# Performance work log

Hardware: AMD Instinct MI355X
Metric: run time of the kernel (lower is better)

The kernel has to match this reference:

```python
import jax, jax.numpy as jnp
import numpy as np
from functools import partial

D_MODEL, D_STATE, D_CONV, EXPAND = 1024, 16, 4, 2
D_INNER = D_MODEL * EXPAND
B_SZ, L = 4, 2048


def setup_inputs() -> dict:
    key = jax.random.key(0)
    ks = jax.random.split(key, 8)
    s = 0.02
    A_init = jnp.log(jnp.arange(1, D_STATE + 1, dtype=jnp.float32))
    return {
        "x": jax.random.normal(ks[0], (B_SZ, L, D_MODEL), jnp.float32),
        "norm_w": jnp.ones((D_MODEL,), jnp.float32),
        "norm_b": jnp.zeros((D_MODEL,), jnp.float32),
        "W_in": jax.random.normal(ks[1], (D_MODEL, 2 * D_INNER), jnp.float32) * s,
        "conv_w": jax.random.normal(ks[2], (D_INNER, 1, D_CONV), jnp.float32) * 0.3,
        "conv_b": jnp.zeros((D_INNER,), jnp.float32),
        "A_log": jnp.broadcast_to(A_init, (D_INNER, D_STATE)).copy(),
        "W_b": jax.random.normal(ks[3], (D_INNER, D_STATE), jnp.float32) * s,
        "W_c": jax.random.normal(ks[4], (D_INNER, D_STATE), jnp.float32) * s,
        "W_delta": jax.random.normal(ks[5], (D_INNER, D_INNER), jnp.float32) * s,
        "b_delta": jnp.zeros((D_INNER,), jnp.float32),
        "D_param": jnp.ones((D_INNER,), jnp.float32),
        "W_out": jax.random.normal(ks[6], (D_INNER, D_MODEL), jnp.float32) * s,
    }


def _layernorm(x, w, b, eps=1e-5):
    mu = jnp.mean(x, axis=-1, keepdims=True)
    var = jnp.mean(jnp.square(x - mu), axis=-1, keepdims=True)
    return (x - mu) * jax.lax.rsqrt(var + eps) * w + b


def reference(x, norm_w, norm_b, W_in, conv_w, conv_b, A_log, W_b, W_c,
              W_delta, b_delta, D_param, W_out):
    residual = x
    xn = _layernorm(x, norm_w, norm_b)
    xz = jnp.einsum('bld,de->ble', xn, W_in)  # [B, L, 2*D_inner]
    x_path, z = jnp.split(xz, 2, axis=-1)

    # depthwise causal conv1d (torch pads both sides K-1 then slices [:L] == left-pad K-1)
    xc = jnp.moveaxis(x_path, 1, 2)  # [B, D_inner, L]
    xc = jax.lax.conv_general_dilated(
        xc, conv_w, window_strides=(1,), padding=[(D_CONV - 1, 0)],
        dimension_numbers=('NCH', 'OIH', 'NCH'), feature_group_count=D_INNER)
    xc = xc + conv_b[None, :, None]
    x_path = jax.nn.silu(jnp.moveaxis(xc, 2, 1))  # [B, L, D_inner]

    Bm = jnp.einsum('bld,dn->bln', x_path, W_b)   # [B, L, N]
    Cm = jnp.einsum('bld,dn->bln', x_path, W_c)   # [B, L, N]
    delta = jax.nn.softplus(jnp.einsum('bld,de->ble', x_path, W_delta) + b_delta)
    A = -jnp.exp(A_log)  # [D_inner, N]

    def step(h, inp):
        xt, dt, Bt, Ct = inp  # xt,dt: [B,D]; Bt,Ct: [B,N]
        A_bar = jnp.exp(dt[..., None] * A)              # [B, D, N]
        h = A_bar * h + (dt * xt)[..., None] * Bt[:, None, :]
        y = jnp.einsum('bdn,bn->bd', h, Ct) + D_param * xt
        return h, y

    h0 = jnp.zeros((x.shape[0], D_INNER, D_STATE), x_path.dtype)
    xs = (jnp.moveaxis(x_path, 1, 0), jnp.moveaxis(delta, 1, 0),
          jnp.moveaxis(Bm, 1, 0), jnp.moveaxis(Cm, 1, 0))
    _, ys = jax.lax.scan(step, h0, xs)           # ys: [L, B, D_inner]
    y = jnp.moveaxis(ys, 0, 1)                   # [B, L, D_inner]

    return jnp.einsum('bld,de->ble', y * jax.nn.silu(z), W_out) + residual
```

## Files before the change

### kernel.cpp

```cpp
#include <hip/hip_runtime.h>
#include <hip/hip_bf16.h>

#define D_MODEL 1024
#define D_STATE 16
#define D_INNER 2048
#define BSZ     4
#define SEQ     2048
#define NTOK    (BSZ*SEQ)
#define NCH     16
#define TC      128

typedef __attribute__((ext_vector_type(8))) short short8;
typedef __attribute__((ext_vector_type(4))) float floatx4;

__device__ __forceinline__ ushort bf2us(float f)
{
    union { __hip_bfloat16 h; ushort u; } c;
    c.h = __float2bfloat16(f);
    return c.u;
}
__device__ __forceinline__ float us2f(ushort u)
{
    union { uint u; float f; } c;
    c.u = ((uint)u) << 16;
    return c.f;
}
__device__ __forceinline__ uint pk2(float a, float b)
{
    return (uint)bf2us(a) | ((uint)bf2us(b) << 16);
}
__device__ __forceinline__ float blo(uint u) { return __uint_as_float(u << 16); }
__device__ __forceinline__ float bhi(uint u) { return __uint_as_float(u & 0xffff0000u); }
__device__ __forceinline__ float softplus_f(float v)
{
    return (v > 20.f) ? v : __logf(1.f + __expf(v));
}

__device__ __forceinline__ void load_lds16(const __hip_bfloat16* g, __hip_bfloat16* l)
{
    __builtin_amdgcn_global_load_lds(
        (const __attribute__((address_space(1))) char*)g,
        (__attribute__((address_space(3))) char*)l, 16, 0, 0);
}

__global__ __launch_bounds__(256) void ln_kernel(
    const float* __restrict__ x, const float* __restrict__ w,
    const float* __restrict__ bvec, __hip_bfloat16* __restrict__ out)
{
    int token = blockIdx.x;
    int tid = threadIdx.x;
    const float4 v = ((const float4*)(x + (size_t)token * D_MODEL))[tid];
    float s  = v.x + v.y + v.z + v.w;
    float sq = v.x*v.x + v.y*v.y + v.z*v.z + v.w*v.w;
#pragma unroll
    for (int o = 32; o; o >>= 1) { s += __shfl_down(s, o, 64); sq += __shfl_down(sq, o, 64); }
    __shared__ float red[8];
    int wid = tid >> 6;
    if ((tid & 63) == 0) { red[wid] = s; red[wid + 4] = sq; }
    __syncthreads();
    s  = red[0] + red[1] + red[2] + red[3];
    sq = red[4] + red[5] + red[6] + red[7];
    float mu  = s * (1.f / D_MODEL);
    float var = sq * (1.f / D_MODEL) - mu * mu;
    float rs  = rsqrtf(var + 1e-5f);
    float4 wv = ((const float4*)w)[tid];
    float4 bv = ((const float4*)bvec)[tid];
    union { ushort4 u; __hip_bfloat16 h[4]; } p;
    p.h[0] = __float2bfloat16((v.x - mu) * rs * wv.x + bv.x);
    p.h[1] = __float2bfloat16((v.y - mu) * rs * wv.y + bv.y);
    p.h[2] = __float2bfloat16((v.z - mu) * rs * wv.z + bv.z);
    p.h[3] = __float2bfloat16((v.w - mu) * rs * wv.w + bv.w);
    ((ushort4*)(out + (size_t)token * D_MODEL))[tid] = p.u;
}

__device__ __forceinline__ void tr_body(
    const float* __restrict__ src, __hip_bfloat16* __restrict__ dst,
    int R, int C, int dstStride, int dstRowOff, int bx, int by, int tx, int ty)
{
    __shared__ float tile[32][33];
#pragma unroll
    for (int i = 0; i < 4; ++i) {
        int r = by * 32 + ty + i * 8;
        int c = bx * 32 + tx;
        if (r < R && c < C) tile[ty + i * 8][tx] = src[(size_t)r * C + c];
    }
    __syncthreads();
#pragma unroll
    for (int i = 0; i < 4; ++i) {
        int c = bx * 32 + ty + i * 8;
        int r = by * 32 + tx;
        if (c < C && r < R)
            dst[(size_t)(dstRowOff + c) * dstStride + r] = __float2bfloat16(tile[tx][ty + i * 8]);
    }
}

__global__ __launch_bounds__(256) void transpose_cast(
    const float* __restrict__ src, __hip_bfloat16* __restrict__ dst,
    int R, int C, int dstStride, int dstRowOff)
{
    tr_body(src, dst, R, C, dstStride, dstRowOff,
            blockIdx.x, blockIdx.y, threadIdx.x, threadIdx.y);
}

__global__ __launch_bounds__(256) void prep_w(
    const float* __restrict__ W_in, const float* __restrict__ W_delta,
    const float* __restrict__ W_b, const float* __restrict__ W_c,
    __hip_bfloat16* __restrict__ wT1, __hip_bfloat16* __restrict__ wT2)
{
    int s = blockIdx.x;
    int tx = threadIdx.x, ty = threadIdx.y;
    if (s < 4096) {
        tr_body(W_in, wT1, 1024, 4096, 1024, 0, s & 127, s >> 7, tx, ty);
    } else if (s < 8192) {
        int q = s - 4096;
        tr_body(W_delta, wT2, 2048, 2048, 2048, 0, q & 63, q >> 6, tx, ty);
    } else if (s < 8256) {
        tr_body(W_b, wT2, 2048, 16, 2048, 2048, 0, s - 8192, tx, ty);
    } else if (s < 8320) {
        tr_body(W_c, wT2, 2048, 16, 2048, 2064, 0, s - 8256, tx, ty);
    } else {
        int i = (s - 8320) * 256 + ty * 32 + tx;
        uint4 z = {0, 0, 0, 0};
        ((uint4*)(wT2 + (size_t)2080 * 2048))[i] = z;
    }
}


#define G256_STG_A(kt_, pb_) do { \
    const __hip_bfloat16* s_ = Ag + (size_t)(kt_) * 64; \
    __hip_bfloat16* d_ = &As[pb_][wv * 512]; \
    load_lds16(s_,                   d_); \
    load_lds16(s_ + (size_t)64 * K,  d_ + 4096); \
    load_lds16(s_ + (size_t)128 * K, d_ + 8192); \
    load_lds16(s_ + (size_t)192 * K, d_ + 12288); \
} while (0)

#define G256_STG_B(kt_, pb_) do { \
    const __hip_bfloat16* s_ = Bg + (size_t)(kt_) * 64; \
    __hip_bfloat16* d_ = &Bs[pb_][wv * 512]; \
    load_lds16(s_,                   d_); \
    load_lds16(s_ + (size_t)64 * K,  d_ + 4096); \
    load_lds16(s_ + (size_t)128 * K, d_ + 8192); \
    load_lds16(s_ + (size_t)192 * K, d_ + 12288); \
} while (0)

#define G256_PHASE(mih_, nih_, ...) do { \
    short8 af_[4][2], bf_[2][2]; \
    _Pragma("unroll") \
    for (int mi4 = 0; mi4 < 4; ++mi4) \
      _Pragma("unroll") \
      for (int kk = 0; kk < 2; ++kk) \
        af_[mi4][kk] = *(const short8*)&As[p][((wm * 128 + ((mih_)*4 + mi4) * 16 + lr) << 6) \
                                             + ((lq ^ (kk << 2) ^ (lr & 7)) << 3)]; \
    _Pragma("unroll") \
    for (int ni2 = 0; ni2 < 2; ++ni2) \
      _Pragma("unroll") \
      for (int kk = 0; kk < 2; ++kk) \
        bf_[ni2][kk] = *(const short8*)&Bs[p][((wn * 64 + ((nih_)*2 + ni2) * 16 + lr) << 6) \
                                             + ((lq ^ (kk << 2) ^ (lr & 7)) << 3)]; \
    __VA_ARGS__; \
    __builtin_amdgcn_s_barrier(); \
    __builtin_amdgcn_s_setprio(1); \
    _Pragma("unroll") \
    for (int kk = 0; kk < 2; ++kk) \
      _Pragma("unroll") \
      for (int mi4 = 0; mi4 < 4; ++mi4) \
        _Pragma("unroll") \
        for (int ni2 = 0; ni2 < 2; ++ni2) \
          acc[(mih_)*4 + mi4][(nih_)*2 + ni2] = __builtin_amdgcn_mfma_f32_16x16x32_bf16( \
              af_[mi4][kk], bf_[ni2][kk], acc[(mih_)*4 + mi4][(nih_)*2 + ni2], 0, 0, 0); \
    __builtin_amdgcn_s_setprio(0); \
    __builtin_amdgcn_s_barrier(); \
} while (0)

template <int MODE, int K>
__device__ __forceinline__ void gemm256_body(
    const __hip_bfloat16* __restrict__ A, const __hip_bfloat16* __restrict__ BT,
    __hip_bfloat16* __restrict__ out1, __hip_bfloat16* __restrict__ out2,
    const float* __restrict__ extra)
{
    __shared__ __align__(16) __hip_bfloat16 As[2][256 * 64];
    __shared__ __align__(16) __hip_bfloat16 Bs[2][256 * 64];
    const int tid = threadIdx.x;
    const int wv = tid >> 6, lane = tid & 63;
    const int wm = wv >> 2, wn = wv & 3;
    const int lr = lane & 15, lq = lane >> 4;
    const int m0 = blockIdx.x * 256, n0 = blockIdx.y * 256;
    const int srow8 = lane >> 3;
    const int scg = (lane & 7) ^ srow8;
    const __hip_bfloat16* Ag = A  + (size_t)(m0 + wv * 8 + srow8) * K + scg * 8;
    const __hip_bfloat16* Bg = BT + (size_t)(n0 + wv * 8 + srow8) * K + scg * 8;

    floatx4 acc[8][4] = {};
    constexpr int NT = K / 64;

    G256_STG_A(0, 0);
    G256_STG_B(0, 0);
    asm volatile("s_waitcnt vmcnt(0)" ::: "memory");
    __builtin_amdgcn_s_barrier();

#pragma unroll 2
    for (int kt = 0; kt < NT; ++kt) {
        const int p = kt & 1;
        const bool pf = (kt + 1 < NT);
        G256_PHASE(0, 0, if (pf) G256_STG_A(kt + 1, p ^ 1));
        G256_PHASE(0, 1, if (pf) G256_STG_B(kt + 1, p ^ 1));
        G256_PHASE(1, 0, (void)0);
        G256_PHASE(1, 1, (void)0);
        asm volatile("s_waitcnt vmcnt(0)" ::: "memory");
        __builtin_amdgcn_s_barrier();
    }

#pragma unroll
    for (int mi = 0; mi < 8; ++mi)
#pragma unroll
        for (int ni = 0; ni < 4; ++ni)
#pragma unroll
            for (int r = 0; r < 4; ++r) {
                int rg = m0 + wm * 128 + mi * 16 + lq * 4 + r;
                int cg = n0 + wn * 64 + ni * 16 + lr;
                float v = acc[mi][ni][r];
                if (MODE == 1) {
                    if (cg < D_INNER) {
                        out1[(size_t)rg * D_INNER + cg] = __float2bfloat16(v);
                    } else {
                        float sv = v / (1.f + __expf(-v));
                        out2[(size_t)rg * D_INNER + (cg - D_INNER)] = __float2bfloat16(sv);
                    }
                } else {
                    out1[(size_t)rg * D_INNER + cg] = __float2bfloat16(softplus_f(v + extra[cg]));
                }
            }
}

__global__ __launch_bounds__(512, 2) void gemm256_xz(
    const __hip_bfloat16* __restrict__ A, const __hip_bfloat16* __restrict__ BT,
    __hip_bfloat16* __restrict__ o1, __hip_bfloat16* __restrict__ o2)
{ gemm256_body<1, 1024>(A, BT, o1, o2, nullptr); }

__global__ __launch_bounds__(512, 2) void gemm256_dt(
    const __hip_bfloat16* __restrict__ A, const __hip_bfloat16* __restrict__ BT,
    __hip_bfloat16* __restrict__ o1, const float* __restrict__ extra)
{ gemm256_body<2, 2048>(A, BT, o1, nullptr, extra); }

template <int MODE>
__device__ __forceinline__ void gemm_body(
    const __hip_bfloat16* __restrict__ A, const __hip_bfloat16* __restrict__ BT,
    int M, int N, int K,
    float* __restrict__ outF,
    __hip_bfloat16* __restrict__ outB1, __hip_bfloat16* __restrict__ outB2,
    const float* __restrict__ extra)
{
    __shared__ __align__(16) __hip_bfloat16 As[128 * 64];
    __shared__ __align__(16) __hip_bfloat16 Bs[128 * 64];
    int tid = threadIdx.x;
    int m0 = blockIdx.x * 128;
    int n0 = blockIdx.y * 128;
    int wv = tid >> 6, lane = tid & 63;
    int wm = (wv >> 1) * 64, wn = (wv & 1) * 64;
    int lr = lane & 15, lq = lane >> 4;

    int srow = wv * 8 + (lane >> 3);
    int scg  = (lane & 7) ^ (lane >> 3);
    const __hip_bfloat16* Ag = A  + (size_t)(m0 + srow) * K + scg * 8;
    const __hip_bfloat16* Bg = BT + (size_t)(n0 + srow) * K + scg * 8;
    __hip_bfloat16* AsW = As + (wv * 8) * 64;
    __hip_bfloat16* BsW = Bs + (wv * 8) * 64;

    int swz = lq ^ (lr & 7);

    floatx4 acc[4][4] = {};

    for (int k0 = 0; k0 < K; k0 += 64) {
        __syncthreads();
#pragma unroll
        for (int i = 0; i < 4; ++i) {
            load_lds16(Ag + (size_t)(i * 32) * K + k0, AsW + i * 32 * 64);
            load_lds16(Bg + (size_t)(i * 32) * K + k0, BsW + i * 32 * 64);
        }
        __syncthreads();
#pragma unroll
        for (int kk = 0; kk < 2; ++kk) {
            int cofs = (swz ^ (kk << 2)) * 8;
            short8 af[4], bf[4];
#pragma unroll
            for (int mi = 0; mi < 4; ++mi)
                af[mi] = *(const short8*)(As + (wm + mi * 16 + lr) * 64 + cofs);
#pragma unroll
            for (int ni = 0; ni < 4; ++ni)
                bf[ni] = *(const short8*)(Bs + (wn + ni * 16 + lr) * 64 + cofs);
#pragma unroll
            for (int mi = 0; mi < 4; ++mi)
#pragma unroll
                for (int ni = 0; ni < 4; ++ni)
                    acc[mi][ni] = __builtin_amdgcn_mfma_f32_16x16x32_bf16(af[mi], bf[ni], acc[mi][ni], 0, 0, 0);
        }
    }

#pragma unroll
    for (int mi = 0; mi < 4; ++mi)
#pragma unroll
        for (int ni = 0; ni < 4; ++ni)
#pragma unroll
            for (int r = 0; r < 4; ++r) {
                int rg = m0 + wm + mi * 16 + lq * 4 + r;
                int cg = n0 + wn + ni * 16 + lr;
                float v = acc[mi][ni][r];
                (void)outB1; (void)outB2;
                outF[(size_t)rg * D_MODEL + cg] = v + extra[(size_t)rg * D_MODEL + cg];
            }
}

__global__ __launch_bounds__(256) void gemm_out(
    const __hip_bfloat16* __restrict__ A, const __hip_bfloat16* __restrict__ BT,
    int M, int N, int K, float* __restrict__ outF,
    __hip_bfloat16* __restrict__ o1, __hip_bfloat16* __restrict__ o2,
    const float* __restrict__ extra)
{ gemm_body<3>(A, BT, M, N, K, outF, o1, o2, extra); }

__global__ __launch_bounds__(256) void gemm_bc(
    const __hip_bfloat16* __restrict__ xp, const __hip_bfloat16* __restrict__ wbc,
    float* __restrict__ part)
{
    __shared__ __align__(16) __hip_bfloat16 As[128 * 64];
    __shared__ __align__(16) __hip_bfloat16 Bs[32 * 64];
    int tid = threadIdx.x, wv = tid >> 6, lane = tid & 63;
    int lr = lane & 15, lq = lane >> 4;
    int m0 = blockIdx.x * 128;
    int k0s = blockIdx.y * 512;
    int srow8 = lane >> 3, scg = (lane & 7) ^ srow8;
    const __hip_bfloat16* Ag = xp  + (size_t)(m0 + wv * 8 + srow8) * 2048 + k0s + scg * 8;
    const __hip_bfloat16* Bg = wbc + (size_t)(wv * 8 + srow8) * 2048 + k0s + scg * 8;
    floatx4 acc[2][2] = {};
    for (int k0 = 0; k0 < 512; k0 += 64) {
        __syncthreads();
#pragma unroll
        for (int i = 0; i < 4; ++i)
            load_lds16(Ag + (size_t)(i * 32) * 2048 + k0, As + (wv * 8 + i * 32) * 64);
        if (wv < 4) load_lds16(Bg + k0, Bs + wv * 8 * 64);
        __syncthreads();
#pragma unroll
        for (int kk = 0; kk < 2; ++kk) {
            int cofs = (lq ^ (kk << 2) ^ (lr & 7)) * 8;
            short8 a0 = *(const short8*)(As + (wv * 32 + lr) * 64 + cofs);
            short8 a1 = *(const short8*)(As + (wv * 32 + 16 + lr) * 64 + cofs);
            short8 b0 = *(const short8*)(Bs + (lr) * 64 + cofs);
            short8 b1 = *(const short8*)(Bs + (16 + lr) * 64 + cofs);
            acc[0][0] = __builtin_amdgcn_mfma_f32_16x16x32_bf16(a0, b0, acc[0][0], 0, 0, 0);
            acc[0][1] = __builtin_amdgcn_mfma_f32_16x16x32_bf16(a0, b1, acc[0][1], 0, 0, 0);
            acc[1][0] = __builtin_amdgcn_mfma_f32_16x16x32_bf16(a1, b0, acc[1][0], 0, 0, 0);
            acc[1][1] = __builtin_amdgcn_mfma_f32_16x16x32_bf16(a1, b1, acc[1][1], 0, 0, 0);
        }
    }
    float* pb = part + (size_t)blockIdx.y * (NTOK * 32);
#pragma unroll
    for (int mi = 0; mi < 2; ++mi)
#pragma unroll
        for (int ni = 0; ni < 2; ++ni)
#pragma unroll
            for (int r = 0; r < 4; ++r)
                pb[(size_t)(m0 + wv * 32 + mi * 16 + lq * 4 + r) * 32 + ni * 16 + lr] = acc[mi][ni][r];
}

__global__ __launch_bounds__(256) void cvt_bc(
    const float* __restrict__ part, ushort* __restrict__ out)
{
    int i = blockIdx.x * 256 + threadIdx.x;
    const float4* p = (const float4*)part;
    float4 a = p[i], b = p[i + 65536], c = p[i + 131072], d = p[i + 196608];
    ushort4 o;
    o.x = bf2us(a.x + b.x + c.x + d.x);
    o.y = bf2us(a.y + b.y + c.y + d.y);
    o.z = bf2us(a.z + b.z + c.z + d.z);
    o.w = bf2us(a.w + b.w + c.w + d.w);
    ((ushort4*)out)[i] = o;
}

__global__ __launch_bounds__(256) void conv_silu(
    const __hip_bfloat16* __restrict__ xin, const float* __restrict__ cw,
    const float* __restrict__ cb, __hip_bfloat16* __restrict__ xp)
{
    int gid = blockIdx.x * 256 + threadIdx.x;
    int d = gid & (D_INNER - 1);
    int rest = gid >> 11;
    int b = rest & 3;
    int ch = rest >> 2;
    int t0 = ch * 64;
    float w0 = cw[d * 4 + 0], w1 = cw[d * 4 + 1], w2 = cw[d * 4 + 2], w3 = cw[d * 4 + 3];
    float bias = cb[d];
    const __hip_bfloat16* base = xin + (size_t)b * SEQ * D_INNER + d;
    __hip_bfloat16* ob = xp + (size_t)b * SEQ * D_INNER + d;
    float xm3 = (t0 >= 3) ? __bfloat162float(base[(size_t)(t0 - 3) * D_INNER]) : 0.f;
    float xm2 = (t0 >= 2) ? __bfloat162float(base[(size_t)(t0 - 2) * D_INNER]) : 0.f;
    float xm1 = (t0 >= 1) ? __bfloat162float(base[(size_t)(t0 - 1) * D_INNER]) : 0.f;
#pragma unroll 4
    for (int t = t0; t < t0 + 64; ++t) {
        float xcur = __bfloat162float(base[(size_t)t * D_INNER]);
        float v = bias + w0 * xm3 + w1 * xm2 + w2 * xm1 + w3 * xcur;
        float sv = v / (1.f + __expf(-v));
        ob[(size_t)t * D_INNER] = __float2bfloat16(sv);
        xm3 = xm2; xm2 = xm1; xm1 = xcur;
    }
}


#define LOAD_A16() \
    const float4* Ar = (const float4*)(A_log + (size_t)d * D_STATE); \
    float4 aA = Ar[0], aB = Ar[1], aC = Ar[2], aD = Ar[3]; \
    float A0 = -__expf(aA.x), A1 = -__expf(aA.y), A2 = -__expf(aA.z), A3 = -__expf(aA.w); \
    float A4 = -__expf(aB.x), A5 = -__expf(aB.y), A6 = -__expf(aB.z), A7 = -__expf(aB.w); \
    float A8 = -__expf(aC.x), A9 = -__expf(aC.y), A10 = -__expf(aC.z), A11 = -__expf(aC.w); \
    float A12 = -__expf(aD.x), A13 = -__expf(aD.y), A14 = -__expf(aD.z), A15 = -__expf(aD.w)

#define UNPACK16(P, r0, r1) \
    float P##0 = blo(r0.x), P##1 = bhi(r0.x), P##2 = blo(r0.y), P##3 = bhi(r0.y); \
    float P##4 = blo(r0.z), P##5 = bhi(r0.z), P##6 = blo(r0.w), P##7 = bhi(r0.w); \
    float P##8 = blo(r1.x), P##9 = bhi(r1.x), P##10 = blo(r1.y), P##11 = bhi(r1.y); \
    float P##12 = blo(r1.z), P##13 = bhi(r1.z), P##14 = blo(r1.w), P##15 = bhi(r1.w)

#define SCAN_STEP_B() do { \
    float dtx = dt * xt; \
    h0  = __expf(dt * A0)  * h0  + dtx * B0; \
    h1  = __expf(dt * A1)  * h1  + dtx * B1; \
    h2  = __expf(dt * A2)  * h2  + dtx * B2; \
    h3  = __expf(dt * A3)  * h3  + dtx * B3; \
    h4  = __expf(dt * A4)  * h4  + dtx * B4; \
    h5  = __expf(dt * A5)  * h5  + dtx * B5; \
    h6  = __expf(dt * A6)  * h6  + dtx * B6; \
    h7  = __expf(dt * A7)  * h7  + dtx * B7; \
    h8  = __expf(dt * A8)  * h8  + dtx * B8; \
    h9  = __expf(dt * A9)  * h9  + dtx * B9; \
    h10 = __expf(dt * A10) * h10 + dtx * B10; \
    h11 = __expf(dt * A11) * h11 + dtx * B11; \
    h12 = __expf(dt * A12) * h12 + dtx * B12; \
    h13 = __expf(dt * A13) * h13 + dtx * B13; \
    h14 = __expf(dt * A14) * h14 + dtx * B14; \
    h15 = __expf(dt * A15) * h15 + dtx * B15; \
} while (0)

__global__ __launch_bounds__(256) void scan_p1(
    const ushort* __restrict__ dtb, const ushort* __restrict__ xpb,
    const ushort* __restrict__ BC, const float* __restrict__ A_log,
    ushort* __restrict__ hloc, ushort* __restrict__ prod)
{
    int gid = blockIdx.x * 256 + threadIdx.x;
    int d  = gid & (D_INNER - 1);
    int ch = (gid >> 11) & (NCH - 1);
    int b  = gid >> 15;
    LOAD_A16();
    float h0 = 0.f, h1 = 0.f, h2 = 0.f, h3 = 0.f, h4 = 0.f, h5 = 0.f, h6 = 0.f, h7 = 0.f;
    float h8 = 0.f, h9 = 0.f, h10 = 0.f, h11 = 0.f, h12 = 0.f, h13 = 0.f, h14 = 0.f, h15 = 0.f;
    float dtsum = 0.f;
    size_t mBase = (size_t)b * SEQ + (size_t)ch * TC;
    const ushort* dtp = dtb + mBase * D_INNER + d;
    const ushort* xpp = xpb + mBase * D_INNER + d;
    const uint4*  bcp = (const uint4*)(BC + mBase * 32);
    float dt = us2f(dtp[0]);
    float xt = us2f(xpp[0]);
    uint4 r0 = bcp[0], r1 = bcp[1];
    for (int t = 0; t < TC - 1; ++t) {
        float dt_n = us2f(dtp[(size_t)(t + 1) * D_INNER]);
        float xt_n = us2f(xpp[(size_t)(t + 1) * D_INNER]);
        uint4 r0_n = bcp[(t + 1) * 4 + 0];
        uint4 r1_n = bcp[(t + 1) * 4 + 1];
        {
            UNPACK16(B, r0, r1);
            dtsum += dt;
            SCAN_STEP_B();
        }
        dt = dt_n; xt = xt_n; r0 = r0_n; r1 = r1_n;
    }
    {
        UNPACK16(B, r0, r1);
        dtsum += dt;
        SCAN_STEP_B();
    }
    size_t idx = ((size_t)(b * NCH + ch) * D_INNER + d) * D_STATE;
    uint4 ho, h2v, po, p2v;
    ho.x  = pk2(h0, h1);   ho.y  = pk2(h2, h3);
    ho.z  = pk2(h4, h5);   ho.w  = pk2(h6, h7);
    h2v.x = pk2(h8, h9);   h2v.y = pk2(h10, h11);
    h2v.z = pk2(h12, h13); h2v.w = pk2(h14, h15);
    po.x  = pk2(__expf(dtsum * A0),  __expf(dtsum * A1));
    po.y  = pk2(__expf(dtsum * A2),  __expf(dtsum * A3));
    po.z  = pk2(__expf(dtsum * A4),  __expf(dtsum * A5));
    po.w  = pk2(__expf(dtsum * A6),  __expf(dtsum * A7));
    p2v.x = pk2(__expf(dtsum * A8),  __expf(dtsum * A9));
    p2v.y = pk2(__expf(dtsum * A10), __expf(dtsum * A11));
    p2v.z = pk2(__expf(dtsum * A12), __expf(dtsum * A13));
    p2v.w = pk2(__expf(dtsum * A14), __expf(dtsum * A15));
    ((uint4*)(hloc + idx))[0] = ho; ((uint4*)(hloc + idx))[1] = h2v;
    ((uint4*)(prod + idx))[0] = po; ((uint4*)(prod + idx))[1] = p2v;
}

__global__ __launch_bounds__(256) void scan_p2(
    const ushort* __restrict__ dtb, const ushort* __restrict__ xpb,
    const ushort* __restrict__ BC, const float* __restrict__ A_log,
    const float* __restrict__ D_param, const ushort* __restrict__ hloc,
    const ushort* __restrict__ prod, ushort* __restrict__ zio)
{
    int gid = blockIdx.x * 256 + threadIdx.x;
    int d  = gid & (D_INNER - 1);
    int ch = (gid >> 11) & (NCH - 1);
    int b  = gid >> 15;
    LOAD_A16();
    float Dp = D_param[d];
    float h0 = 0.f, h1 = 0.f, h2 = 0.f, h3 = 0.f, h4 = 0.f, h5 = 0.f, h6 = 0.f, h7 = 0.f;
    float h8 = 0.f, h9 = 0.f, h10 = 0.f, h11 = 0.f, h12 = 0.f, h13 = 0.f, h14 = 0.f, h15 = 0.f;
    for (int j = 0; j < ch; ++j) {
        size_t jdx = ((size_t)(b * NCH + j) * D_INNER + d) * D_STATE;
        uint4 a0 = ((const uint4*)(hloc + jdx))[0];
        uint4 a1 = ((const uint4*)(hloc + jdx))[1];
        uint4 q0 = ((const uint4*)(prod + jdx))[0];
        uint4 q1 = ((const uint4*)(prod + jdx))[1];
        h0  = blo(a0.x) + blo(q0.x) * h0;   h1  = bhi(a0.x) + bhi(q0.x) * h1;
        h2  = blo(a0.y) + blo(q0.y) * h2;   h3  = bhi(a0.y) + bhi(q0.y) * h3;
        h4  = blo(a0.z) + blo(q0.z) * h4;   h5  = bhi(a0.z) + bhi(q0.z) * h5;
        h6  = blo(a0.w) + blo(q0.w) * h6;   h7  = bhi(a0.w) + bhi(q0.w) * h7;
        h8  = blo(a1.x) + blo(q1.x) * h8;   h9  = bhi(a1.x) + bhi(q1.x) * h9;
        h10 = blo(a1.y) + blo(q1.y) * h10;  h11 = bhi(a1.y) + bhi(q1.y) * h11;
        h12 = blo(a1.z) + blo(q1.z) * h12;  h13 = bhi(a1.z) + bhi(q1.z) * h13;
        h14 = blo(a1.w) + blo(q1.w) * h14;  h15 = bhi(a1.w) + bhi(q1.w) * h15;
    }
    size_t mBase = (size_t)b * SEQ + (size_t)ch * TC;
    const ushort* dtp = dtb + mBase * D_INNER + d;
    const ushort* xpp = xpb + mBase * D_INNER + d;
    const uint4*  bcp = (const uint4*)(BC + mBase * 32);
    ushort* zp = zio + mBase * D_INNER + d;
    float dt = us2f(dtp[0]);
    float xt = us2f(xpp[0]);
    uint4 r0 = bcp[0], r1 = bcp[1], r2 = bcp[2], r3 = bcp[3];
    for (int t = 0; t < TC; ++t) {
        float dt_n = 0.f, xt_n = 0.f;
        uint4 r0_n = {0,0,0,0}, r1_n = {0,0,0,0}, r2_n = {0,0,0,0}, r3_n = {0,0,0,0};
        if (t < TC - 1) {
            dt_n = us2f(dtp[(size_t)(t + 1) * D_INNER]);
            xt_n = us2f(xpp[(size_t)(t + 1) * D_INNER]);
            r0_n = bcp[(t + 1) * 4 + 0];
            r1_n = bcp[(t + 1) * 4 + 1];
            r2_n = bcp[(t + 1) * 4 + 2];
            r3_n = bcp[(t + 1) * 4 + 3];
        }
        {
            UNPACK16(B, r0, r1);
            UNPACK16(C, r2, r3);
            float dtx = dt * xt;
            float y = Dp * xt;
            h0  = __expf(dt * A0)  * h0  + dtx * B0;   y += h0  * C0;
            h1  = __expf(dt * A1)  * h1  + dtx * B1;   y += h1  * C1;
            h2  = __expf(dt * A2)  * h2  + dtx * B2;   y += h2  * C2;
            h3  = __expf(dt * A3)  * h3  + dtx * B3;   y += h3  * C3;
            h4  = __expf(dt * A4)  * h4  + dtx * B4;   y += h4  * C4;
            h5  = __expf(dt * A5)  * h5  + dtx * B5;   y += h5  * C5;
            h6  = __expf(dt * A6)  * h6  + dtx * B6;   y += h6  * C6;
            h7  = __expf(dt * A7)  * h7  + dtx * B7;   y += h7  * C7;
            h8  = __expf(dt * A8)  * h8  + dtx * B8;   y += h8  * C8;
            h9  = __expf(dt * A9)  * h9  + dtx * B9;   y += h9  * C9;
            h10 = __expf(dt * A10) * h10 + dtx * B10;  y += h10 * C10;
            h11 = __expf(dt * A11) * h11 + dtx * B11;  y += h11 * C11;
            h12 = __expf(dt * A12) * h12 + dtx * B12;  y += h12 * C12;
            h13 = __expf(dt * A13) * h13 + dtx * B13;  y += h13 * C13;
            h14 = __expf(dt * A14) * h14 + dtx * B14;  y += h14 * C14;
            h15 = __expf(dt * A15) * h15 + dtx * B15;  y += h15 * C15;
            float z = us2f(zp[(size_t)t * D_INNER]);
            zp[(size_t)t * D_INNER] = bf2us(y * z);
        }
        dt = dt_n; xt = xt_n; r0 = r0_n; r1 = r1_n; r2 = r2_n; r3 = r3_n;
    }
}

extern "C" void kernel_launch(void* const* d_in, const int* in_sizes, int n_in,
                              void* d_out, int out_size, void* d_ws, size_t ws_size,
                              hipStream_t stream)
{
    const float* x       = (const float*)d_in[0];
    const float* norm_w  = (const float*)d_in[1];
    const float* norm_b  = (const float*)d_in[2];
    const float* W_in    = (const float*)d_in[3];
    const float* conv_w  = (const float*)d_in[4];
    const float* conv_b  = (const float*)d_in[5];
    const float* A_log   = (const float*)d_in[6];
    const float* W_b     = (const float*)d_in[7];
    const float* W_c     = (const float*)d_in[8];
    const float* W_delta = (const float*)d_in[9];
    const float* b_delta = (const float*)d_in[10];
    const float* D_param = (const float*)d_in[11];
    const float* W_out   = (const float*)d_in[12];
    float* out = (float*)d_out;

    char* ws = (char*)d_ws;
    char* R1 = ws;
    char* R2 = R1 + (size_t)33554432;
    char* R3 = R2 + (size_t)33554432;
    char* R4 = R3 + (size_t)33554432;
    char* R5 = R4 + (size_t)8912896;

    __hip_bfloat16* xnb  = (__hip_bfloat16*)R1;
    __hip_bfloat16* wT1  = (__hip_bfloat16*)(R1 + 16777216);
    __hip_bfloat16* xp   = (__hip_bfloat16*)R1;
    __hip_bfloat16* xraw = (__hip_bfloat16*)R2;
    float*          BCf  = (float*)R2;
    __hip_bfloat16* dtb  = (__hip_bfloat16*)R2;
    __hip_bfloat16* wT3  = (__hip_bfloat16*)R2;
    __hip_bfloat16* zio  = (__hip_bfloat16*)R3;
    __hip_bfloat16* wT2  = (__hip_bfloat16*)R4;
    ushort*         hloc = (ushort*)R4;
    ushort*         prodb= (ushort*)(R4 + 4194304);
    __hip_bfloat16* BCb  = (__hip_bfloat16*)R5;

    ln_kernel<<<NTOK, 256, 0, stream>>>(x, norm_w, norm_b, xnb);

    prep_w<<<8416, dim3(32, 8), 0, stream>>>(W_in, W_delta, W_b, W_c, wT1, wT2);

    gemm256_xz<<<dim3(32, 16), 512, 0, stream>>>(xnb, wT1, xraw, zio);

    conv_silu<<<1024, 256, 0, stream>>>(xraw, conv_w, conv_b, xp);

    gemm_bc<<<dim3(64, 4), 256, 0, stream>>>(xp, wT2 + (size_t)2048 * 2048, BCf);
    cvt_bc<<<256, 256, 0, stream>>>(BCf, (ushort*)BCb);

    gemm256_dt<<<dim3(32, 8), 512, 0, stream>>>(xp, wT2, dtb, b_delta);

    scan_p1<<<512, 256, 0, stream>>>((const ushort*)dtb, (const ushort*)xp,
                                     (const ushort*)BCb, A_log, hloc, prodb);
    scan_p2<<<512, 256, 0, stream>>>((const ushort*)dtb, (const ushort*)xp,
                                     (const ushort*)BCb, A_log, D_param,
                                     hloc, prodb, (ushort*)zio);

    transpose_cast<<<dim3(32, 64), dim3(32, 8), 0, stream>>>(W_out, wT3, 2048, 1024, 2048, 0);

    gemm_out<<<dim3(NTOK / 128, D_MODEL / 128), 256, 0, stream>>>(
        zio, wT3, NTOK, D_MODEL, 2048, out, nullptr, nullptr, x);

    (void)in_sizes; (void)n_in; (void)out_size; (void)ws_size;
}
```

Baseline: 559.1 us.

## Split scan state across thread pairs and stagger GEMM tile loads by quarter

The chunked selective scan now gives each (batch, channel, chunk) to two threads, each owning 8 of the 16 state dimensions. The two partial outputs are combined with a lane shuffle, which doubles thread count and halves per-thread register and latency-bound work. Separately, the 256x256 GEMM splits its A/B LDS staging into half-tiles issued across all four compute phases with partial vmcnt waits. That replaces the full drain at the end of each k-step and should overlap global loads with MFMA better. The cost is more duplicated per-thread overhead in the scan and finer-grained synchronization reasoning in the GEMM.

```diff
diff --git a/kernel.cpp b/kernel.cpp
--- a/kernel.cpp
+++ b/kernel.cpp
@@ -126,25 +126,24 @@
 }
 
 
-#define G256_STG_A(kt_, pb_) do { \
-    const __hip_bfloat16* s_ = Ag + (size_t)(kt_) * 64; \
-    __hip_bfloat16* d_ = &As[pb_][wv * 512]; \
+#define VMW(n) asm volatile("s_waitcnt vmcnt(" #n ")" ::: "memory")
+
+#define G256_STG_AQ(q_, kt_, pb_) do { \
+    const __hip_bfloat16* s_ = Ag + (size_t)(kt_) * 64 + (size_t)((q_) * 64) * K; \
+    __hip_bfloat16* d_ = &As[pb_][(q_) * 64 * 64 + wv * 512]; \
     load_lds16(s_,                   d_); \
-    load_lds16(s_ + (size_t)64 * K,  d_ + 4096); \
-    load_lds16(s_ + (size_t)128 * K, d_ + 8192); \
-    load_lds16(s_ + (size_t)192 * K, d_ + 12288); \
+    load_lds16(s_ + (size_t)128 * K, d_ + 128 * 64); \
 } while (0)
 
-#define G256_STG_B(kt_, pb_) do { \
-    const __hip_bfloat16* s_ = Bg + (size_t)(kt_) * 64; \
-    __hip_bfloat16* d_ = &Bs[pb_][wv * 512]; \
+#define G256_STG_BQ(q_, kt_, pb_) do { \
+    const int rb_ = ((wv >> 2) * 64) + (q_) * 32 + (wv & 3) * 8; \
+    const __hip_bfloat16* s_ = Bg0 + (size_t)(kt_) * 64 + (size_t)rb_ * K; \
+    __hip_bfloat16* d_ = &Bs[pb_][rb_ * 64]; \
     load_lds16(s_,                   d_); \
-    load_lds16(s_ + (size_t)64 * K,  d_ + 4096); \
-    load_lds16(s_ + (size_t)128 * K, d_ + 8192); \
-    load_lds16(s_ + (size_t)192 * K, d_ + 12288); \
+    load_lds16(s_ + (size_t)128 * K, d_ + 128 * 64); \
 } while (0)
 
-#define G256_PHASE(mih_, nih_, ...) do { \
+#define G256_PHASE(mih_, nih_, STG_, WAIT_) do { \
     short8 af_[4][2], bf_[2][2]; \
     _Pragma("unroll") \
     for (int mi4 = 0; mi4 < 4; ++mi4) \
@@ -158,7 +157,8 @@
       for (int kk = 0; kk < 2; ++kk) \
         bf_[ni2][kk] = *(const short8*)&Bs[p][((wn * 64 + ((nih_)*2 + ni2) * 16 + lr) << 6) \
                                              + ((lq ^ (kk << 2) ^ (lr & 7)) << 3)]; \
-    __VA_ARGS__; \
+    STG_; \
+    WAIT_; \
     __builtin_amdgcn_s_barrier(); \
     __builtin_amdgcn_s_setprio(1); \
     _Pragma("unroll") \
@@ -188,27 +188,30 @@
     const int m0 = blockIdx.x * 256, n0 = blockIdx.y * 256;
     const int srow8 = lane >> 3;
     const int scg = (lane & 7) ^ srow8;
-    const __hip_bfloat16* Ag = A  + (size_t)(m0 + wv * 8 + srow8) * K + scg * 8;
-    const __hip_bfloat16* Bg = BT + (size_t)(n0 + wv * 8 + srow8) * K + scg * 8;
+    const __hip_bfloat16* Ag  = A  + (size_t)(m0 + wv * 8 + srow8) * K + scg * 8;
+    const __hip_bfloat16* Bg0 = BT + (size_t)(n0 + srow8) * K + scg * 8;
 
     floatx4 acc[8][4] = {};
     constexpr int NT = K / 64;
 
-    G256_STG_A(0, 0);
-    G256_STG_B(0, 0);
-    asm volatile("s_waitcnt vmcnt(0)" ::: "memory");
+    G256_STG_AQ(0, 0, 0);
+    G256_STG_BQ(0, 0, 0);
+    G256_STG_AQ(1, 0, 0);
+    G256_STG_BQ(1, 0, 0);
+    VMW(4);
     __builtin_amdgcn_s_barrier();
 
 #pragma unroll 2
     for (int kt = 0; kt < NT; ++kt) {
         const int p = kt & 1;
         const bool pf = (kt + 1 < NT);
-        G256_PHASE(0, 0, if (pf) G256_STG_A(kt + 1, p ^ 1));
-        G256_PHASE(0, 1, if (pf) G256_STG_B(kt + 1, p ^ 1));
-        G256_PHASE(1, 0, (void)0);
-        G256_PHASE(1, 1, (void)0);
-        asm volatile("s_waitcnt vmcnt(0)" ::: "memory");
-        __builtin_amdgcn_s_barrier();
+        G256_PHASE(0, 0, if (pf) G256_STG_AQ(0, kt + 1, p ^ 1),
+                   if (pf) { VMW(4); } else { VMW(2); });
+        G256_PHASE(1, 0, if (pf) G256_STG_BQ(0, kt + 1, p ^ 1),
+                   if (pf) { VMW(4); } else { VMW(0); });
+        G256_PHASE(1, 1, if (pf) G256_STG_AQ(1, kt + 1, p ^ 1), (void)0);
+        G256_PHASE(0, 1, if (pf) G256_STG_BQ(1, kt + 1, p ^ 1),
+                   if (pf) { VMW(4); });
     }
 
 #pragma unroll
@@ -404,38 +407,26 @@
 }
 
 
-#define LOAD_A16() \
-    const float4* Ar = (const float4*)(A_log + (size_t)d * D_STATE); \
-    float4 aA = Ar[0], aB = Ar[1], aC = Ar[2], aD = Ar[3]; \
+#define LOAD_A8() \
+    const float4* Ar = (const float4*)(A_log + (size_t)d * D_STATE) + pi * 2; \
+    float4 aA = Ar[0], aB = Ar[1]; \
     float A0 = -__expf(aA.x), A1 = -__expf(aA.y), A2 = -__expf(aA.z), A3 = -__expf(aA.w); \
-    float A4 = -__expf(aB.x), A5 = -__expf(aB.y), A6 = -__expf(aB.z), A7 = -__expf(aB.w); \
-    float A8 = -__expf(aC.x), A9 = -__expf(aC.y), A10 = -__expf(aC.z), A11 = -__expf(aC.w); \
-    float A12 = -__expf(aD.x), A13 = -__expf(aD.y), A14 = -__expf(aD.z), A15 = -__expf(aD.w)
-
-#define UNPACK16(P, r0, r1) \
-    float P##0 = blo(r0.x), P##1 = bhi(r0.x), P##2 = blo(r0.y), P##3 = bhi(r0.y); \
-    float P##4 = blo(r0.z), P##5 = bhi(r0.z), P##6 = blo(r0.w), P##7 = bhi(r0.w); \
-    float P##8 = blo(r1.x), P##9 = bhi(r1.x), P##10 = blo(r1.y), P##11 = bhi(r1.y); \
-    float P##12 = blo(r1.z), P##13 = bhi(r1.z), P##14 = blo(r1.w), P##15 = bhi(r1.w)
-
-#define SCAN_STEP_B() do { \
+    float A4 = -__expf(aB.x), A5 = -__expf(aB.y), A6 = -__expf(aB.z), A7 = -__expf(aB.w)
+
+#define UNPACK8(P, r) \
+    float P##0 = blo(r.x), P##1 = bhi(r.x), P##2 = blo(r.y), P##3 = bhi(r.y); \
+    float P##4 = blo(r.z), P##5 = bhi(r.z), P##6 = blo(r.w), P##7 = bhi(r.w)
+
+#define SCAN_STEP8() do { \
     float dtx = dt * xt; \
-    h0  = __expf(dt * A0)  * h0  + dtx * B0; \
-    h1  = __expf(dt * A1)  * h1  + dtx * B1; \
-    h2  = __expf(dt * A2)  * h2  + dtx * B2; \
-    h3  = __expf(dt * A3)  * h3  + dtx * B3; \
-    h4  = __expf(dt * A4)  * h4  + dtx * B4; \
-    h5  = __expf(dt * A5)  * h5  + dtx * B5; \
-    h6  = __expf(dt * A6)  * h6  + dtx * B6; \
-    h7  = __expf(dt * A7)  * h7  + dtx * B7; \
-    h8  = __expf(dt * A8)  * h8  + dtx * B8; \
-    h9  = __expf(dt * A9)  * h9  + dtx * B9; \
-    h10 = __expf(dt * A10) * h10 + dtx * B10; \
-    h11 = __expf(dt * A11) * h11 + dtx * B11; \
-    h12 = __expf(dt * A12) * h12 + dtx * B12; \
-    h13 = __expf(dt * A13) * h13 + dtx * B13; \
-    h14 = __expf(dt * A14) * h14 + dtx * B14; \
-    h15 = __expf(dt * A15) * h15 + dtx * B15; \
+    h0 = __expf(dt * A0) * h0 + dtx * B0; \
+    h1 = __expf(dt * A1) * h1 + dtx * B1; \
+    h2 = __expf(dt * A2) * h2 + dtx * B2; \
+    h3 = __expf(dt * A3) * h3 + dtx * B3; \
+    h4 = __expf(dt * A4) * h4 + dtx * B4; \
+    h5 = __expf(dt * A5) * h5 + dtx * B5; \
+    h6 = __expf(dt * A6) * h6 + dtx * B6; \
+    h7 = __expf(dt * A7) * h7 + dtx * B7; \
 } while (0)
 
 __global__ __launch_bounds__(256) void scan_p1(
@@ -444,53 +435,47 @@
     ushort* __restrict__ hloc, ushort* __restrict__ prod)
 {
     int gid = blockIdx.x * 256 + threadIdx.x;
-    int d  = gid & (D_INNER - 1);
-    int ch = (gid >> 11) & (NCH - 1);
-    int b  = gid >> 15;
-    LOAD_A16();
+    int pi = gid & 1;
+    int pr = gid >> 1;
+    int d  = pr & (D_INNER - 1);
+    int ch = (pr >> 11) & (NCH - 1);
+    int b  = pr >> 15;
+    LOAD_A8();
     float h0 = 0.f, h1 = 0.f, h2 = 0.f, h3 = 0.f, h4 = 0.f, h5 = 0.f, h6 = 0.f, h7 = 0.f;
-    float h8 = 0.f, h9 = 0.f, h10 = 0.f, h11 = 0.f, h12 = 0.f, h13 = 0.f, h14 = 0.f, h15 = 0.f;
     float dtsum = 0.f;
     size_t mBase = (size_t)b * SEQ + (size_t)ch * TC;
     const ushort* dtp = dtb + mBase * D_INNER + d;
     const ushort* xpp = xpb + mBase * D_INNER + d;
-    const uint4*  bcp = (const uint4*)(BC + mBase * 32);
+    const uint4*  bcp = (const uint4*)(BC + mBase * 32) + pi;
     float dt = us2f(dtp[0]);
     float xt = us2f(xpp[0]);
-    uint4 r0 = bcp[0], r1 = bcp[1];
+    uint4 r0 = bcp[0];
     for (int t = 0; t < TC - 1; ++t) {
         float dt_n = us2f(dtp[(size_t)(t + 1) * D_INNER]);
         float xt_n = us2f(xpp[(size_t)(t + 1) * D_INNER]);
-        uint4 r0_n = bcp[(t + 1) * 4 + 0];
-        uint4 r1_n = bcp[(t + 1) * 4 + 1];
+        uint4 r0_n = bcp[(t + 1) * 4];
         {
-            UNPACK16(B, r0, r1);
+            UNPACK8(B, r0);
             dtsum += dt;
-            SCAN_STEP_B();
+            SCAN_STEP8();
         }
-        dt = dt_n; xt = xt_n; r0 = r0_n; r1 = r1_n;
+        dt = dt_n; xt = xt_n; r0 = r0_n;
     }
     {
-        UNPACK16(B, r0, r1);
+        UNPACK8(B, r0);
         dtsum += dt;
-        SCAN_STEP_B();
+        SCAN_STEP8();
     }
     size_t idx = ((size_t)(b * NCH + ch) * D_INNER + d) * D_STATE;
-    uint4 ho, h2v, po, p2v;
-    ho.x  = pk2(h0, h1);   ho.y  = pk2(h2, h3);
-    ho.z  = pk2(h4, h5);   ho.w  = pk2(h6, h7);
-    h2v.x = pk2(h8, h9);   h2v.y = pk2(h10, h11);
-    h2v.z = pk2(h12, h13); h2v.w = pk2(h14, h15);
-    po.x  = pk2(__expf(dtsum * A0),  __expf(dtsum * A1));
-    po.y  = pk2(__expf(dtsum * A2),  __expf(dtsum * A3));
-    po.z  = pk2(__expf(dtsum * A4),  __expf(dtsum * A5));
-    po.w  = pk2(__expf(dtsum * A6),  __expf(dtsum * A7));
-    p2v.x = pk2(__expf(dtsum * A8),  __expf(dtsum * A9));
-    p2v.y = pk2(__expf(dtsum * A10), __expf(dtsum * A11));
-    p2v.z = pk2(__expf(dtsum * A12), __expf(dtsum * A13));
-    p2v.w = pk2(__expf(dtsum * A14), __expf(dtsum * A15));
-    ((uint4*)(hloc + idx))[0] = ho; ((uint4*)(hloc + idx))[1] = h2v;
-    ((uint4*)(prod + idx))[0] = po; ((uint4*)(prod + idx))[1] = p2v;
+    uint4 ho, po;
+    ho.x = pk2(h0, h1); ho.y = pk2(h2, h3);
+    ho.z = pk2(h4, h5); ho.w = pk2(h6, h7);
+    po.x = pk2(__expf(dtsum * A0), __expf(dtsum * A1));
+    po.y = pk2(__expf(dtsum * A2), __expf(dtsum * A3));
+    po.z = pk2(__expf(dtsum * A4), __expf(dtsum * A5));
+    po.w = pk2(__expf(dtsum * A6), __expf(dtsum * A7));
+    ((uint4*)(hloc + idx))[pi] = ho;
+    ((uint4*)(prod + idx))[pi] = po;
 }
 
 __global__ __launch_bounds__(256) void scan_p2(
@@ -500,72 +485,59 @@
     const ushort* __restrict__ prod, ushort* __restrict__ zio)
 {
     int gid = blockIdx.x * 256 + threadIdx.x;
-    int d  = gid & (D_INNER - 1);
-    int ch = (gid >> 11) & (NCH - 1);
-    int b  = gid >> 15;
-    LOAD_A16();
+    int pi = gid & 1;
+    int pr = gid >> 1;
+    int d  = pr & (D_INNER - 1);
+    int ch = (pr >> 11) & (NCH - 1);
+    int b  = pr >> 15;
+    LOAD_A8();
     float Dp = D_param[d];
     float h0 = 0.f, h1 = 0.f, h2 = 0.f, h3 = 0.f, h4 = 0.f, h5 = 0.f, h6 = 0.f, h7 = 0.f;
-    float h8 = 0.f, h9 = 0.f, h10 = 0.f, h11 = 0.f, h12 = 0.f, h13 = 0.f, h14 = 0.f, h15 = 0.f;
     for (int j = 0; j < ch; ++j) {
         size_t jdx = ((size_t)(b * NCH + j) * D_INNER + d) * D_STATE;
-        uint4 a0 = ((const uint4*)(hloc + jdx))[0];
-        uint4 a1 = ((const uint4*)(hloc + jdx))[1];
-        uint4 q0 = ((const uint4*)(prod + jdx))[0];
-        uint4 q1 = ((const uint4*)(prod + jdx))[1];
-        h0  = blo(a0.x) + blo(q0.x) * h0;   h1  = bhi(a0.x) + bhi(q0.x) * h1;
-        h2  = blo(a0.y) + blo(q0.y) * h2;   h3  = bhi(a0.y) + bhi(q0.y) * h3;
-        h4  = blo(a0.z) + blo(q0.z) * h4;   h5  = bhi(a0.z) + bhi(q0.z) * h5;
-        h6  = blo(a0.w) + blo(q0.w) * h6;   h7  = bhi(a0.w) + bhi(q0.w) * h7;
-        h8  = blo(a1.x) + blo(q1.x) * h8;   h9  = bhi(a1.x) + bhi(q1.x) * h9;
-        h10 = blo(a1.y) + blo(q1.y) * h10;  h11 = bhi(a1.y) + bhi(q1.y) * h11;
-        h12 = blo(a1.z) + blo(q1.z) * h12;  h13 = bhi(a1.z) + bhi(q1.z) * h13;
-        h14 = blo(a1.w) + blo(q1.w) * h14;  h15 = bhi(a1.w) + bhi(q1.w) * h15;
+        uint4 a0 = ((const uint4*)(hloc + jdx))[pi];
+        uint4 q0 = ((const uint4*)(prod + jdx))[pi];
+        h0 = blo(a0.x) + blo(q0.x) * h0;   h1 = bhi(a0.x) + bhi(q0.x) * h1;
+        h2 = blo(a0.y) + blo(q0.y) * h2;   h3 = bhi(a0.y) + bhi(q0.y) * h3;
+        h4 = blo(a0.z) + blo(q0.z) * h4;   h5 = bhi(a0.z) + bhi(q0.z) * h5;
+        h6 = blo(a0.w) + blo(q0.w) * h6;   h7 = bhi(a0.w) + bhi(q0.w) * h7;
     }
     size_t mBase = (size_t)b * SEQ + (size_t)ch * TC;
     const ushort* dtp = dtb + mBase * D_INNER + d;
     const ushort* xpp = xpb + mBase * D_INNER + d;
-    const uint4*  bcp = (const uint4*)(BC + mBase * 32);
+    const uint4*  bcp = (const uint4*)(BC + mBase * 32) + pi;
     ushort* zp = zio + mBase * D_INNER + d;
     float dt = us2f(dtp[0]);
     float xt = us2f(xpp[0]);
-    uint4 r0 = bcp[0], r1 = bcp[1], r2 = bcp[2], r3 = bcp[3];
+    uint4 rB = bcp[0], rC = bcp[2];
     for (int t = 0; t < TC; ++t) {
         float dt_n = 0.f, xt_n = 0.f;
-        uint4 r0_n = {0,0,0,0}, r1_n = {0,0,0,0}, r2_n = {0,0,0,0}, r3_n = {0,0,0,0};
+        uint4 rB_n = {0,0,0,0}, rC_n = {0,0,0,0};
         if (t < TC - 1) {
             dt_n = us2f(dtp[(size_t)(t + 1) * D_INNER]);
             xt_n = us2f(xpp[(size_t)(t + 1) * D_INNER]);
-            r0_n = bcp[(t + 1) * 4 + 0];
-            r1_n = bcp[(t + 1) * 4 + 1];
-            r2_n = bcp[(t + 1) * 4 + 2];
-            r3_n = bcp[(t + 1) * 4 + 3];
+            rB_n = bcp[(t + 1) * 4];
+            rC_n = bcp[(t + 1) * 4 + 2];
         }
         {
-            UNPACK16(B, r0, r1);
-            UNPACK16(C, r2, r3);
+            UNPACK8(B, rB);
+            UNPACK8(C, rC);
             float dtx = dt * xt;
-            float y = Dp * xt;
-            h0  = __expf(dt * A0)  * h0  + dtx * B0;   y += h0  * C0;
-            h1  = __expf(dt * A1)  * h1  + dtx * B1;   y += h1  * C1;
-            h2  = __expf(dt * A2)  * h2  + dtx * B2;   y += h2  * C2;
-            h3  = __expf(dt * A3)  * h3  + dtx * B3;   y += h3  * C3;
-            h4  = __expf(dt * A4)  * h4  + dtx * B4;   y += h4  * C4;
-            h5  = __expf(dt * A5)  * h5  + dtx * B5;   y += h5  * C5;
-            h6  = __expf(dt * A6)  * h6  + dtx * B6;   y += h6  * C6;
-            h7  = __expf(dt * A7)  * h7  + dtx * B7;   y += h7  * C7;
-            h8  = __expf(dt * A8)  * h8  + dtx * B8;   y += h8  * C8;
-            h9  = __expf(dt * A9)  * h9  + dtx * B9;   y += h9  * C9;
-            h10 = __expf(dt * A10) * h10 + dtx * B10;  y += h10 * C10;
-            h11 = __expf(dt * A11) * h11 + dtx * B11;  y += h11 * C11;
-            h12 = __expf(dt * A12) * h12 + dtx * B12;  y += h12 * C12;
-            h13 = __expf(dt * A13) * h13 + dtx * B13;  y += h13 * C13;
-            h14 = __expf(dt * A14) * h14 + dtx * B14;  y += h14 * C14;
-            h15 = __expf(dt * A15) * h15 + dtx * B15;  y += h15 * C15;
+            float y = pi ? 0.f : Dp * xt;
+            h0 = __expf(dt * A0) * h0 + dtx * B0;   y += h0 * C0;
+            h1 = __expf(dt * A1) * h1 + dtx * B1;   y += h1 * C1;
+            h2 = __expf(dt * A2) * h2 + dtx * B2;   y += h2 * C2;
+            h3 = __expf(dt * A3) * h3 + dtx * B3;   y += h3 * C3;
+            h4 = __expf(dt * A4) * h4 + dtx * B4;   y += h4 * C4;
+            h5 = __expf(dt * A5) * h5 + dtx * B5;   y += h5 * C5;
+            h6 = __expf(dt * A6) * h6 + dtx * B6;   y += h6 * C6;
+            h7 = __expf(dt * A7) * h7 + dtx * B7;   y += h7 * C7;
+            float ys = y + __shfl_xor(y, 1);
             float z = us2f(zp[(size_t)t * D_INNER]);
-            zp[(size_t)t * D_INNER] = bf2us(y * z);
+            if (pi == 0)
+                zp[(size_t)t * D_INNER] = bf2us(ys * z);
         }
-        dt = dt_n; xt = xt_n; r0 = r0_n; r1 = r1_n; r2 = r2_n; r3 = r3_n;
+        dt = dt_n; xt = xt_n; rB = rB_n; rC = rC_n;
     }
 }
 
@@ -621,11 +593,11 @@
 
     gemm256_dt<<<dim3(32, 8), 512, 0, stream>>>(xp, wT2, dtb, b_delta);
 
-    scan_p1<<<512, 256, 0, stream>>>((const ushort*)dtb, (const ushort*)xp,
-                                     (const ushort*)BCb, A_log, hloc, prodb);
-    scan_p2<<<512, 256, 0, stream>>>((const ushort*)dtb, (const ushort*)xp,
-                                     (const ushort*)BCb, A_log, D_param,
-                                     hloc, prodb, (ushort*)zio);
+    scan_p1<<<1024, 256, 0, stream>>>((const ushort*)dtb, (const ushort*)xp,
+                                      (const ushort*)BCb, A_log, hloc, prodb);
+    scan_p2<<<1024, 256, 0, stream>>>((const ushort*)dtb, (const ushort*)xp,
+                                      (const ushort*)BCb, A_log, D_param,
+                                      hloc, prodb, (ushort*)zio);
 
     transpose_cast<<<dim3(32, 64), dim3(32, 8), 0, stream>>>(W_out, wT3, 2048, 1024, 2048, 0);
 
```

Result: slower. 571.5 us (+2.2%).
